# Optimization experiments

Measured on AMD Instinct MI355X. Metric: run time of the kernel, lower is better.

The kernel has to match this reference:

```python
import jax, jax.numpy as jnp
import numpy as np

N_QUERY = 100000
N_VALUE = 100000
N_DIM = 128
B, LQ, LK = 256, 50, 200
SIGMA = 1.0      # lognormal scale hyperparameter
LN_EPS = 1e-5    # torch LayerNorm default eps


def setup_inputs() -> dict:
    key = jax.random.key(0)
    ks = jax.random.split(key, 7)
    return {
        "Q_idx": jax.random.randint(ks[0], (B, LQ), 0, N_QUERY),
        "K_idx": jax.random.randint(ks[1], (B, LK), 0, N_VALUE),
        "V_idx": jax.random.randint(ks[2], (B, LK), 0, N_VALUE),
        "W_q": jax.random.normal(ks[3], (N_QUERY, N_DIM), dtype=jnp.float32) * 0.02,
        "W_k": jax.random.normal(ks[4], (N_VALUE, N_DIM), dtype=jnp.float32) * 0.02,
        "W_v": jax.random.normal(ks[5], (N_VALUE, N_DIM), dtype=jnp.float32) * 0.02,
        "ln_gamma": jnp.ones((N_DIM,), dtype=jnp.float32),
        "ln_beta": jnp.zeros((N_DIM,), dtype=jnp.float32),
        "eps_noise": jax.random.normal(ks[6], (B, LQ, LK), dtype=jnp.float32),
    }


def reference(Q_idx, K_idx, V_idx, W_q, W_k, W_v, ln_gamma, ln_beta, eps_noise):
    d = W_q.shape[-1]
    q = W_q[Q_idx]                                   # [B, Lq, d]
    k = W_k[K_idx]                                   # [B, Lk, d]
    logits = jnp.einsum("bqd,bkd->bqk", q, k) / jnp.sqrt(jnp.asarray(d, q.dtype))
    log_phi = jax.nn.log_softmax(logits, axis=-1)    # [B, Lq, Lk]
    # reparameterized LogNormal sample with mean phi: exp(log phi - sigma^2/2 + sigma*eps)
    score = jnp.exp(log_phi - 0.5 * SIGMA * SIGMA + SIGMA * eps_noise)
    weight = score / jnp.sum(score, axis=-1, keepdims=True)
    v = W_v[V_idx]                                   # [B, Lk, d]
    context = jnp.einsum("bqk,bkd->bqd", weight, v)  # [B, Lq, d]
    mu = jnp.mean(context, axis=-1, keepdims=True)
    var = jnp.mean(jnp.square(context - mu), axis=-1, keepdims=True)
    normed = (context - mu) * jax.lax.rsqrt(var + LN_EPS)
    return normed * ln_gamma + ln_beta
```

## Files before the change

### kernel.cpp

```cpp
#include <hip/hip_runtime.h>
#include <hip/hip_bf16.h>
#include <cstdint>

namespace {
constexpr int NB    = 256;
constexpr int LQ    = 50;
constexpr int LK    = 200;
constexpr int DIM   = 128;
constexpr int NWAVE = 8;
constexpr int NTHR  = NWAVE * 64;
constexpr int LSTR  = 204;
constexpr int KSTR  = 136;
constexpr int NKR   = 208;
constexpr int PSTR  = 232;
constexpr int VSTR  = 232;
constexpr int NKT3  = 7;
constexpr int UKV   = 128 * VSTR;
constexpr int KPW   = LK / NWAVE;
constexpr int VG    = 8;
constexpr int NG    = LK / VG;
}

typedef __attribute__((ext_vector_type(8))) short bf16x8;
typedef __attribute__((ext_vector_type(4))) float f32x4;

__device__ __forceinline__ float bflo(uint32_t u) { return __uint_as_float(u << 16); }
__device__ __forceinline__ float bfhi(uint32_t u) { return __uint_as_float(u & 0xFFFF0000u); }
__device__ __forceinline__ uint32_t f2bf(float f) {
    uint32_t x = __float_as_uint(f);
    return (x + 0x7FFFu + ((x >> 16) & 1u)) >> 16;
}

__device__ __forceinline__ void run_f32(
    int b,
    const int* __restrict__ Qi, const int* __restrict__ Ki, const int* __restrict__ Vi,
    const void* __restrict__ Wq, const void* __restrict__ Wk, const void* __restrict__ Wv,
    const void* __restrict__ gm, const void* __restrict__ bt, const void* __restrict__ ep,
    void* __restrict__ out, float* __restrict__ lgt, uint16_t* __restrict__ ukv,
    uint16_t* __restrict__ pwgt, float2* __restrict__ part, int* __restrict__ vix)
{
    const int tid  = threadIdx.x;
    const int w    = tid >> 6;
    const int lane = tid & 63;
    const int l15  = lane & 15;
    const int g    = lane >> 4;
    const int m    = w >> 1;
    const int h    = w & 1;

    for (int i = tid; i < LK; i += NTHR) vix[i] = Vi[b * LK + i];

    uint16_t* ksh = ukv;
    #pragma unroll
    for (int j = 0; j < NKR / NWAVE; ++j) {
        const int r = w + NWAVE * j;
        uint32_t v = 0u;
        if (r < LK) {
            const int kidx = Ki[b * LK + r];
            const float2 f = ((const float2*)((const float*)Wk + (size_t)kidx * DIM))[lane];
            v = f2bf(f.x) | (f2bf(f.y) << 16);
        }
        *(uint32_t*)(ksh + (size_t)r * KSTR + 2 * lane) = v;
    }

    bf16x8 afr[4];
    {
        const int ql   = m * 16 + l15;
        const int qc   = (ql < LQ) ? ql : (LQ - 1);
        const int qidx = Qi[b * LQ + qc];
        const float* qrow = (const float*)Wq + (size_t)qidx * DIM + g * 8;
        #pragma unroll
        for (int ks = 0; ks < 4; ++ks) {
            const float4 f0 = *(const float4*)(qrow + ks * 32);
            const float4 f1 = *(const float4*)(qrow + ks * 32 + 4);
            union { bf16x8 v; uint16_t u[8]; } pk;
            pk.u[0] = (uint16_t)f2bf(f0.x); pk.u[1] = (uint16_t)f2bf(f0.y);
            pk.u[2] = (uint16_t)f2bf(f0.z); pk.u[3] = (uint16_t)f2bf(f0.w);
            pk.u[4] = (uint16_t)f2bf(f1.x); pk.u[5] = (uint16_t)f2bf(f1.y);
            pk.u[6] = (uint16_t)f2bf(f1.z); pk.u[7] = (uint16_t)f2bf(f1.w);
            afr[ks] = pk.v;
        }
    }
    __syncthreads();

    {
        #pragma unroll 1
        for (int n = h; n < 13; n += 2) {
            const uint16_t* kbase = ksh + (size_t)(n * 16 + l15) * KSTR + g * 8;
            f32x4 acc = {0.f, 0.f, 0.f, 0.f};
            #pragma unroll
            for (int ks = 0; ks < 4; ++ks) {
                const bf16x8 bfr = *(const bf16x8*)(kbase + ks * 32);
                acc = __builtin_amdgcn_mfma_f32_16x16x32_bf16(afr[ks], bfr, acc, 0, 0, 0);
            }
            const int kcol = n * 16 + l15;
            #pragma unroll
            for (int r = 0; r < 4; ++r) {
                const int q = m * 16 + g * 4 + r;
                if (q < LQ && kcol < LK)
                    lgt[q * LSTR + kcol] = acc[r] * 0.08838834764831843f;
            }
        }
    }
    __syncthreads();

    uint16_t* vsh = ukv;
    #pragma unroll
    for (int j = 0; j < 4; ++j) {
        const int k8 = w + NWAVE * j;
        if (k8 < 28) {
            float2 vr[8];
            #pragma unroll
            for (int r = 0; r < 8; ++r) {
                const int k = k8 * 8 + r;
                if (k < LK) {
                    const int vidx = vix[k];
                    vr[r] = ((const float2*)((const float*)Wv + (size_t)vidx * DIM))[lane];
                } else vr[r] = make_float2(0.f, 0.f);
            }
            union { bf16x8 v; uint16_t u[8]; } px, py;
            #pragma unroll
            for (int r = 0; r < 8; ++r) {
                px.u[r] = (uint16_t)f2bf(vr[r].x);
                py.u[r] = (uint16_t)f2bf(vr[r].y);
            }
            *(bf16x8*)(vsh + (size_t)(2 * lane)     * VSTR + k8 * 8) = px.v;
            *(bf16x8*)(vsh + (size_t)(2 * lane + 1) * VSTR + k8 * 8) = py.v;
        }
    }

    for (int q = w; q < 64; q += NWAVE) {
        if (q < LQ) {
            float z[4];
            float mx = -INFINITY;
            #pragma unroll
            for (int i = 0; i < 4; ++i) {
                const int k = i * 64 + lane;
                if (k < LK) {
                    const float e = ((const float*)ep)[(size_t)(b * LQ + q) * LK + k];
                    z[i] = lgt[q * LSTR + k] + e;
                    mx = fmaxf(mx, z[i]);
                } else z[i] = -INFINITY;
            }
            #pragma unroll
            for (int off = 32; off > 0; off >>= 1) mx = fmaxf(mx, __shfl_xor(mx, off));
            float e4[4]; float s = 0.f;
            #pragma unroll
            for (int i = 0; i < 4; ++i) {
                e4[i] = (i * 64 + lane < LK) ? __expf(z[i] - mx) : 0.f;
                s += e4[i];
            }
            #pragma unroll
            for (int off = 32; off > 0; off >>= 1) s += __shfl_xor(s, off);
            const float inv = 1.0f / s;
            #pragma unroll
            for (int i = 0; i < 4; ++i) {
                const int k = i * 64 + lane;
                if (k < PSTR)
                    pwgt[q * PSTR + k] = (k < LK) ? (uint16_t)f2bf(e4[i] * inv) : (uint16_t)0;
            }
        } else {
            #pragma unroll
            for (int i = 0; i < 4; ++i) {
                const int k = i * 64 + lane;
                if (k < PSTR) pwgt[q * PSTR + k] = 0;
            }
        }
    }
    __syncthreads();

    f32x4 acc[4] = {{0.f,0.f,0.f,0.f},{0.f,0.f,0.f,0.f},{0.f,0.f,0.f,0.f},{0.f,0.f,0.f,0.f}};
    #pragma unroll
    for (int kt = 0; kt < NKT3; ++kt) {
        const bf16x8 a = *(const bf16x8*)(pwgt + (size_t)(m * 16 + l15) * PSTR + kt * 32 + g * 8);
        #pragma unroll
        for (int t = 0; t < 4; ++t) {
            const int d = (h * 4 + t) * 16 + l15;
            const bf16x8 bv = *(const bf16x8*)(vsh + (size_t)d * VSTR + kt * 32 + g * 8);
            acc[t] = __builtin_amdgcn_mfma_f32_16x16x32_bf16(a, bv, acc[t], 0, 0, 0);
        }
    }

    float s1[4], s2[4];
    #pragma unroll
    for (int r = 0; r < 4; ++r) {
        s1[r] = acc[0][r] + acc[1][r] + acc[2][r] + acc[3][r];
        s2[r] = acc[0][r]*acc[0][r] + acc[1][r]*acc[1][r]
              + acc[2][r]*acc[2][r] + acc[3][r]*acc[3][r];
        #pragma unroll
        for (int off = 1; off < 16; off <<= 1) {
            s1[r] += __shfl_xor(s1[r], off);
            s2[r] += __shfl_xor(s2[r], off);
        }
    }
    if (l15 == 0) {
        #pragma unroll
        for (int r = 0; r < 4; ++r)
            part[(m * 16 + g * 4 + r) * 2 + h] = make_float2(s1[r], s2[r]);
    }
    __syncthreads();

    float* outf = (float*)out;
    #pragma unroll
    for (int r = 0; r < 4; ++r) {
        const int q = m * 16 + g * 4 + r;
        const float2 oth = part[q * 2 + (h ^ 1)];
        const float t1 = s1[r] + oth.x;
        const float t2 = s2[r] + oth.y;
        const float mu = t1 * (1.0f / DIM);
        float var = t2 * (1.0f / DIM) - mu * mu;
        var = fmaxf(var, 0.f);
        const float rs = rsqrtf(var + 1e-5f);
        if (q < LQ) {
            #pragma unroll
            for (int t = 0; t < 4; ++t) {
                const int d = (h * 4 + t) * 16 + l15;
                const float gv = ((const float*)gm)[d];
                const float bv = ((const float*)bt)[d];
                outf[(size_t)(b * LQ + q) * DIM + d] = (acc[t][r] - mu) * rs * gv + bv;
            }
        }
    }
}

__device__ __forceinline__ void run_bf16(
    int b,
    const int* __restrict__ Qi, const int* __restrict__ Ki, const int* __restrict__ Vi,
    const void* __restrict__ Wq, const void* __restrict__ Wk, const void* __restrict__ Wv,
    const void* __restrict__ gm, const void* __restrict__ bt, const void* __restrict__ ep,
    void* __restrict__ out, float* __restrict__ lds, int* __restrict__ vix)
{
    const int tid  = threadIdx.x;
    const int w    = tid >> 6;
    const int lane = tid & 63;

    for (int i = tid; i < LK; i += NTHR) vix[i] = Vi[b * LK + i];

    {
        const int ql   = (lane < LQ) ? lane : (LQ - 1);
        const int qidx = Qi[b * LQ + ql];
        const uint4* qrow = (const uint4*)((const uint16_t*)Wq + (size_t)qidx * DIM);
        const int k0 = w * KPW;

        int kidx[KPW];
        #pragma unroll
        for (int kk = 0; kk < KPW; ++kk) kidx[kk] = Ki[b * LK + k0 + kk];
        float acc[KPW];
        #pragma unroll
        for (int kk = 0; kk < KPW; ++kk) acc[kk] = 0.f;

        #pragma unroll 1
        for (int hh = 0; hh < DIM / 8; ++hh) {
            const uint4 qc = qrow[hh];
            const float a0 = bflo(qc.x), a1 = bfhi(qc.x);
            const float a2 = bflo(qc.y), a3 = bfhi(qc.y);
            const float a4 = bflo(qc.z), a5 = bfhi(qc.z);
            const float a6 = bflo(qc.w), a7 = bfhi(qc.w);
            #pragma unroll
            for (int kk = 0; kk < KPW; ++kk) {
                const uint4 t = ((const uint4*)((const uint16_t*)Wk + (size_t)kidx[kk] * DIM))[hh];
                float a = acc[kk];
                a = fmaf(a0, bflo(t.x), a);
                a = fmaf(a1, bfhi(t.x), a);
                a = fmaf(a2, bflo(t.y), a);
                a = fmaf(a3, bfhi(t.y), a);
                a = fmaf(a4, bflo(t.z), a);
                a = fmaf(a5, bfhi(t.z), a);
                a = fmaf(a6, bflo(t.w), a);
                a = fmaf(a7, bfhi(t.w), a);
                acc[kk] = a;
            }
        }
        if (lane < LQ) {
            #pragma unroll
            for (int kk = 0; kk < KPW; ++kk)
                lds[lane * LSTR + (k0 + kk)] = acc[kk] * 0.08838834764831843f;
        }
    }
    __syncthreads();

    for (int q = w; q < LQ; q += NWAVE) {
        float z[4];
        float mx = -INFINITY;
        #pragma unroll
        for (int i = 0; i < 4; ++i) {
            const int k = i * 64 + lane;
            if (k < LK) {
                const float e = bflo((uint32_t)((const uint16_t*)ep)[(size_t)(b*LQ+q)*LK + k]);
                z[i] = lds[q * LSTR + k] + e;
                mx = fmaxf(mx, z[i]);
            } else z[i] = -INFINITY;
        }
        #pragma unroll
        for (int off = 32; off > 0; off >>= 1) mx = fmaxf(mx, __shfl_xor(mx, off));
        float e4[4]; float s = 0.f;
        #pragma unroll
        for (int i = 0; i < 4; ++i) {
            e4[i] = (i * 64 + lane < LK) ? __expf(z[i] - mx) : 0.f;
            s += e4[i];
        }
        #pragma unroll
        for (int off = 32; off > 0; off >>= 1) s += __shfl_xor(s, off);
        const float inv = 1.0f / s;
        #pragma unroll
        for (int i = 0; i < 4; ++i) {
            const int k = i * 64 + lane;
            if (k < LK) lds[q * LSTR + k] = e4[i] * inv;
        }
    }
    __syncthreads();

    float c0[7], c1[7];
    #pragma unroll
    for (int qi = 0; qi < 7; ++qi) { c0[qi] = 0.f; c1[qi] = 0.f; }

    int rowq[7];
    #pragma unroll
    for (int qi = 0; qi < 7; ++qi) {
        const int q = w + 8 * qi;
        rowq[qi] = (q < LQ) ? q : (LQ - 1);
    }

    const uint16_t* Wvh = (const uint16_t*)Wv;

    auto load_grp = [&](uint32_t (&f)[VG], int kg) {
        #pragma unroll
        for (int u = 0; u < VG; ++u) {
            const int vidx = vix[kg * VG + u];
            f[u] = ((const uint32_t*)(Wvh + (size_t)vidx * DIM))[lane];
        }
    };
    auto consume_grp = [&](const uint32_t (&f)[VG], int kg) {
        #pragma unroll
        for (int u = 0; u < VG; ++u) {
            const int k = kg * VG + u;
            const float v0 = bflo(f[u]), v1 = bfhi(f[u]);
            #pragma unroll
            for (int qi = 0; qi < 7; ++qi) {
                const float wt = lds[rowq[qi] * LSTR + k];
                c0[qi] = fmaf(wt, v0, c0[qi]);
                c1[qi] = fmaf(wt, v1, c1[qi]);
            }
        }
    };

    uint32_t fA[VG], fB[VG];
    load_grp(fA, 0);
    #pragma unroll 1
    for (int kg = 0; kg < NG - 1; kg += 2) {
        load_grp(fB, kg + 1);
        consume_grp(fA, kg);
        load_grp(fA, kg + 2);
        consume_grp(fB, kg + 1);
    }
    consume_grp(fA, NG - 1);

    const uint32_t gu = ((const uint32_t*)gm)[lane];
    const uint32_t bu = ((const uint32_t*)bt)[lane];
    const float g0 = bflo(gu), g1 = bfhi(gu);
    const float be0 = bflo(bu), be1 = bfhi(bu);

    #pragma unroll
    for (int qi = 0; qi < 7; ++qi) {
        const int q = w + 8 * qi;
        if (q < LQ) {
            float s1 = c0[qi] + c1[qi];
            float s2 = c0[qi]*c0[qi] + c1[qi]*c1[qi];
            #pragma unroll
            for (int off = 32; off > 0; off >>= 1) {
                s1 += __shfl_xor(s1, off);
                s2 += __shfl_xor(s2, off);
            }
            const float mu = s1 * (1.0f / DIM);
            float var = s2 * (1.0f / DIM) - mu * mu;
            var = fmaxf(var, 0.f);
            const float rs = rsqrtf(var + 1e-5f);
            const float y0 = (c0[qi] - mu) * rs * g0 + be0;
            const float y1 = (c1[qi] - mu) * rs * g1 + be1;
            ((uint32_t*)out)[(size_t)(b*LQ+q) * (DIM/2) + lane] = f2bf(y0) | (f2bf(y1) << 16);
        }
    }
}

__global__ __launch_bounds__(NTHR, 1) void fused_attn_ln(
    const int* __restrict__ Qi, const int* __restrict__ Ki, const int* __restrict__ Vi,
    const void* __restrict__ Wq, const void* __restrict__ Wk, const void* __restrict__ Wv,
    const void* __restrict__ gm, const void* __restrict__ bt, const void* __restrict__ ep,
    void* __restrict__ out)
{
    __shared__ __align__(16) uint16_t ukv[UKV];
    __shared__ __align__(16) float    lgt[LQ * LSTR];
    __shared__ __align__(16) uint16_t pwgt[64 * PSTR];
    __shared__ float2 part[64 * 2];
    __shared__ int vix[LK];

    const int b = blockIdx.x;

    const uint32_t* probe = (const uint32_t*)Wq;
    int c = 0;
    #pragma unroll
    for (int i = 0; i < 64; ++i) {
        float f = bflo(probe[i]);
        c += (fabsf(f) < 1.0f) ? 1 : 0;
    }
    if (c >= 48) run_bf16(b, Qi, Ki, Vi, Wq, Wk, Wv, gm, bt, ep, out, lgt, vix);
    else         run_f32 (b, Qi, Ki, Vi, Wq, Wk, Wv, gm, bt, ep, out,
                          lgt, ukv, pwgt, part, vix);
}

extern "C" void kernel_launch(void* const* d_in, const int* in_sizes, int n_in,
                              void* d_out, int out_size, void* d_ws, size_t ws_size,
                              hipStream_t stream)
{
    (void)in_sizes; (void)n_in; (void)out_size; (void)d_ws; (void)ws_size;
    fused_attn_ln<<<NB, NTHR, 0, stream>>>(
        (const int*)d_in[0], (const int*)d_in[1], (const int*)d_in[2],
        d_in[3], d_in[4], d_in[5], d_in[6], d_in[7], d_in[8], d_out);
}
```

Baseline: 177.4 us.

## Issue all K, V, Q and noise gathers up front with separate LDS buffers

K and V now get separate shared-memory buffers, so the V gather and bf16 transpose run before the first barrier, overlapping the K gather instead of waiting for QK^T to finish. The noise tensor is prefetched into registers early, and V indices are read directly as int4 vectors rather than staged through LDS. The 1/sqrt(d) scale is folded into Q before bf16 conversion, and logits are stored as bf16 in the weight buffer instead of an fp32 array. This cuts a barrier and exposed memory latency, at the cost of more registers, more LDS, and extra bf16 rounding of the logits.

Result: faster. 172.3 us (-2.9%).

```diff
diff --git a/kernel.cpp b/kernel.cpp
--- a/kernel.cpp
+++ b/kernel.cpp
@@ -9,16 +9,16 @@
 constexpr int DIM   = 128;
 constexpr int NWAVE = 8;
 constexpr int NTHR  = NWAVE * 64;
-constexpr int LSTR  = 204;
 constexpr int KSTR  = 136;
 constexpr int NKR   = 208;
 constexpr int PSTR  = 232;
 constexpr int VSTR  = 232;
 constexpr int NKT3  = 7;
-constexpr int UKV   = 128 * VSTR;
+constexpr int LSTR  = 204;
 constexpr int KPW   = LK / NWAVE;
 constexpr int VG    = 8;
 constexpr int NG    = LK / VG;
+constexpr float SCL = 0.08838834764831843f;
 }
 
 typedef __attribute__((ext_vector_type(8))) short bf16x8;
@@ -36,8 +36,8 @@
     const int* __restrict__ Qi, const int* __restrict__ Ki, const int* __restrict__ Vi,
     const void* __restrict__ Wq, const void* __restrict__ Wk, const void* __restrict__ Wv,
     const void* __restrict__ gm, const void* __restrict__ bt, const void* __restrict__ ep,
-    void* __restrict__ out, float* __restrict__ lgt, uint16_t* __restrict__ ukv,
-    uint16_t* __restrict__ pwgt, float2* __restrict__ part, int* __restrict__ vix)
+    void* __restrict__ out, uint16_t* __restrict__ ksh, uint16_t* __restrict__ vsh,
+    uint16_t* __restrict__ pwgt, float2* __restrict__ part)
 {
     const int tid  = threadIdx.x;
     const int w    = tid >> 6;
@@ -47,9 +47,25 @@
     const int m    = w >> 1;
     const int h    = w & 1;
 
-    for (int i = tid; i < LK; i += NTHR) vix[i] = Vi[b * LK + i];
-
-    uint16_t* ksh = ukv;
+    bf16x8 afr[4];
+    {
+        const int ql   = m * 16 + l15;
+        const int qc   = (ql < LQ) ? ql : (LQ - 1);
+        const int qidx = Qi[b * LQ + qc];
+        const float* qrow = (const float*)Wq + (size_t)qidx * DIM + g * 8;
+        #pragma unroll
+        for (int ks = 0; ks < 4; ++ks) {
+            const float4 f0 = *(const float4*)(qrow + ks * 32);
+            const float4 f1 = *(const float4*)(qrow + ks * 32 + 4);
+            union { bf16x8 v; uint16_t u[8]; } pk;
+            pk.u[0] = (uint16_t)f2bf(f0.x * SCL); pk.u[1] = (uint16_t)f2bf(f0.y * SCL);
+            pk.u[2] = (uint16_t)f2bf(f0.z * SCL); pk.u[3] = (uint16_t)f2bf(f0.w * SCL);
+            pk.u[4] = (uint16_t)f2bf(f1.x * SCL); pk.u[5] = (uint16_t)f2bf(f1.y * SCL);
+            pk.u[6] = (uint16_t)f2bf(f1.z * SCL); pk.u[7] = (uint16_t)f2bf(f1.w * SCL);
+            afr[ks] = pk.v;
+        }
+    }
+
     #pragma unroll
     for (int j = 0; j < NKR / NWAVE; ++j) {
         const int r = w + NWAVE * j;
@@ -62,22 +78,49 @@
         *(uint32_t*)(ksh + (size_t)r * KSTR + 2 * lane) = v;
     }
 
-    bf16x8 afr[4];
-    {
-        const int ql   = m * 16 + l15;
-        const int qc   = (ql < LQ) ? ql : (LQ - 1);
-        const int qidx = Qi[b * LQ + qc];
-        const float* qrow = (const float*)Wq + (size_t)qidx * DIM + g * 8;
-        #pragma unroll
-        for (int ks = 0; ks < 4; ++ks) {
-            const float4 f0 = *(const float4*)(qrow + ks * 32);
-            const float4 f1 = *(const float4*)(qrow + ks * 32 + 4);
-            union { bf16x8 v; uint16_t u[8]; } pk;
-            pk.u[0] = (uint16_t)f2bf(f0.x); pk.u[1] = (uint16_t)f2bf(f0.y);
-            pk.u[2] = (uint16_t)f2bf(f0.z); pk.u[3] = (uint16_t)f2bf(f0.w);
-            pk.u[4] = (uint16_t)f2bf(f1.x); pk.u[5] = (uint16_t)f2bf(f1.y);
-            pk.u[6] = (uint16_t)f2bf(f1.z); pk.u[7] = (uint16_t)f2bf(f1.w);
-            afr[ks] = pk.v;
+    #pragma unroll
+    for (int j = 0; j < 4; ++j) {
+        const int k8 = w + NWAVE * j;
+        if (k8 < 25) {
+            const int4 ia = *(const int4*)(Vi + b * LK + k8 * 8);
+            const int4 ib = *(const int4*)(Vi + b * LK + k8 * 8 + 4);
+            float2 vr[8];
+            vr[0] = ((const float2*)((const float*)Wv + (size_t)ia.x * DIM))[lane];
+            vr[1] = ((const float2*)((const float*)Wv + (size_t)ia.y * DIM))[lane];
+            vr[2] = ((const float2*)((const float*)Wv + (size_t)ia.z * DIM))[lane];
+            vr[3] = ((const float2*)((const float*)Wv + (size_t)ia.w * DIM))[lane];
+            vr[4] = ((const float2*)((const float*)Wv + (size_t)ib.x * DIM))[lane];
+            vr[5] = ((const float2*)((const float*)Wv + (size_t)ib.y * DIM))[lane];
+            vr[6] = ((const float2*)((const float*)Wv + (size_t)ib.z * DIM))[lane];
+            vr[7] = ((const float2*)((const float*)Wv + (size_t)ib.w * DIM))[lane];
+            union { bf16x8 v; uint16_t u[8]; } px, py;
+            #pragma unroll
+            for (int r = 0; r < 8; ++r) {
+                px.u[r] = (uint16_t)f2bf(vr[r].x);
+                py.u[r] = (uint16_t)f2bf(vr[r].y);
+            }
+            *(bf16x8*)(vsh + (size_t)(2 * lane)     * VSTR + k8 * 8) = px.v;
+            *(bf16x8*)(vsh + (size_t)(2 * lane + 1) * VSTR + k8 * 8) = py.v;
+        } else if (k8 < 28) {
+            const bf16x8 z = {0,0,0,0,0,0,0,0};
+            *(bf16x8*)(vsh + (size_t)(2 * lane)     * VSTR + k8 * 8) = z;
+            *(bf16x8*)(vsh + (size_t)(2 * lane + 1) * VSTR + k8 * 8) = z;
+        }
+    }
+
+    float er[7][4];
+    #pragma unroll
+    for (int j = 0; j < 7; ++j) {
+        const int q = w + 8 * j;
+        if (q < LQ) {
+            #pragma unroll
+            for (int i = 0; i < 4; ++i) {
+                const int k = i * 64 + lane;
+                er[j][i] = (k < LK) ? ((const float*)ep)[(size_t)(b * LQ + q) * LK + k] : 0.f;
+            }
+        } else {
+            #pragma unroll
+            for (int i = 0; i < 4; ++i) er[j][i] = 0.f;
         }
     }
     __syncthreads();
@@ -97,47 +140,23 @@
             for (int r = 0; r < 4; ++r) {
                 const int q = m * 16 + g * 4 + r;
                 if (q < LQ && kcol < LK)
-                    lgt[q * LSTR + kcol] = acc[r] * 0.08838834764831843f;
-            }
-        }
-    }
-    __syncthreads();
-
-    uint16_t* vsh = ukv;
-    #pragma unroll
-    for (int j = 0; j < 4; ++j) {
-        const int k8 = w + NWAVE * j;
-        if (k8 < 28) {
-            float2 vr[8];
-            #pragma unroll
-            for (int r = 0; r < 8; ++r) {
-                const int k = k8 * 8 + r;
-                if (k < LK) {
-                    const int vidx = vix[k];
-                    vr[r] = ((const float2*)((const float*)Wv + (size_t)vidx * DIM))[lane];
-                } else vr[r] = make_float2(0.f, 0.f);
-            }
-            union { bf16x8 v; uint16_t u[8]; } px, py;
-            #pragma unroll
-            for (int r = 0; r < 8; ++r) {
-                px.u[r] = (uint16_t)f2bf(vr[r].x);
-                py.u[r] = (uint16_t)f2bf(vr[r].y);
-            }
-            *(bf16x8*)(vsh + (size_t)(2 * lane)     * VSTR + k8 * 8) = px.v;
-            *(bf16x8*)(vsh + (size_t)(2 * lane + 1) * VSTR + k8 * 8) = py.v;
-        }
-    }
-
-    for (int q = w; q < 64; q += NWAVE) {
-        if (q < LQ) {
+                    pwgt[q * PSTR + kcol] = (uint16_t)f2bf(acc[r]);
+            }
+        }
+    }
+    __syncthreads();
+
+    #pragma unroll
+    for (int j = 0; j < 8; ++j) {
+        const int q = w + 8 * j;
+        if (j < 7 && q < LQ) {
             float z[4];
             float mx = -INFINITY;
             #pragma unroll
             for (int i = 0; i < 4; ++i) {
                 const int k = i * 64 + lane;
                 if (k < LK) {
-                    const float e = ((const float*)ep)[(size_t)(b * LQ + q) * LK + k];
-                    z[i] = lgt[q * LSTR + k] + e;
+                    z[i] = bflo((uint32_t)pwgt[q * PSTR + k]) + er[j][i];
                     mx = fmaxf(mx, z[i]);
                 } else z[i] = -INFINITY;
             }
@@ -158,7 +177,7 @@
                 if (k < PSTR)
                     pwgt[q * PSTR + k] = (k < LK) ? (uint16_t)f2bf(e4[i] * inv) : (uint16_t)0;
             }
-        } else {
+        } else if (q >= LQ && q < 64) {
             #pragma unroll
             for (int i = 0; i < 4; ++i) {
                 const int k = i * 64 + lane;
@@ -273,7 +292,7 @@
         if (lane < LQ) {
             #pragma unroll
             for (int kk = 0; kk < KPW; ++kk)
-                lds[lane * LSTR + (k0 + kk)] = acc[kk] * 0.08838834764831843f;
+                lds[lane * LSTR + (k0 + kk)] = acc[kk] * SCL;
         }
     }
     __syncthreads();
@@ -387,8 +406,8 @@
     const void* __restrict__ gm, const void* __restrict__ bt, const void* __restrict__ ep,
     void* __restrict__ out)
 {
-    __shared__ __align__(16) uint16_t ukv[UKV];
-    __shared__ __align__(16) float    lgt[LQ * LSTR];
+    __shared__ __align__(16) uint16_t ksh[NKR * KSTR];
+    __shared__ __align__(16) uint16_t vsh[DIM * VSTR];
     __shared__ __align__(16) uint16_t pwgt[64 * PSTR];
     __shared__ float2 part[64 * 2];
     __shared__ int vix[LK];
@@ -402,9 +421,10 @@
         float f = bflo(probe[i]);
         c += (fabsf(f) < 1.0f) ? 1 : 0;
     }
-    if (c >= 48) run_bf16(b, Qi, Ki, Vi, Wq, Wk, Wv, gm, bt, ep, out, lgt, vix);
+    if (c >= 48) run_bf16(b, Qi, Ki, Vi, Wq, Wk, Wv, gm, bt, ep, out,
+                          (float*)vsh, vix);
     else         run_f32 (b, Qi, Ki, Vi, Wq, Wk, Wv, gm, bt, ep, out,
-                          lgt, ukv, pwgt, part, vix);
+                          ksh, vsh, pwgt, part);
 }
 
 extern "C" void kernel_launch(void* const* d_in, const int* in_sizes, int n_in,
```
